# Kernel optimization log

Hardware: AMD Instinct MI355X
Metric: run time of the kernel (lower is better)

Reference implementation:

```python
import jax, jax.numpy as jnp
import numpy as np

NUM_HEADS = 8
EPS = 1e-9


def setup_inputs() -> dict:
    key = jax.random.key(0)
    ks = jax.random.split(key, 5)
    B, S, D = 2, 2048, 512
    x = jax.random.normal(ks[0], (B, S, D), dtype=jnp.float32)
    Wq = jax.random.normal(ks[1], (D, D), dtype=jnp.float32) * (1.0 / np.sqrt(D))
    Wk = jax.random.normal(ks[2], (D, D), dtype=jnp.float32) * (1.0 / np.sqrt(D))
    Wv = jax.random.normal(ks[3], (D, D), dtype=jnp.float32) * (1.0 / np.sqrt(D))
    Wo = jax.random.normal(ks[4], (D, D), dtype=jnp.float32) * (1.0 / np.sqrt(D))
    gamma = jnp.ones((D,), dtype=jnp.float32)
    beta = jnp.zeros((D,), dtype=jnp.float32)
    return {"x": x, "Wq": Wq, "Wk": Wk, "Wv": Wv, "Wo": Wo, "gamma": gamma, "beta": beta}


def _layernorm(x, gamma, beta):
    mean = jnp.mean(x, axis=-1, keepdims=True)
    var = jnp.mean(jnp.square(x - mean), axis=-1, keepdims=True)
    return gamma * ((x - mean) * jax.lax.rsqrt(var + EPS)) + beta


def reference(x, Wq, Wk, Wv, Wo, gamma, beta):
    B, S, D = x.shape
    H = NUM_HEADS
    dh = D // H
    # Note: in the original, K_V=(inputs, inputs) is captured BEFORE LayerNorm,
    # so only Q is layer-normalized; K and V use the raw inputs.
    q_in = _layernorm(x, gamma, beta)
    Q = jnp.einsum('bsd,de->bse', q_in, Wq).reshape(B, S, H, dh)
    K = jnp.einsum('bsd,de->bse', x, Wk).reshape(B, S, H, dh)
    V = jnp.einsum('bsd,de->bse', x, Wv).reshape(B, S, H, dh)
    # scaled dot-product attention (bias = 0, dropout disabled since dropout=1)
    scores = jnp.einsum('bqhd,bkhd->bhqk', Q, K) / jnp.sqrt(jnp.float32(dh))
    attn = jax.nn.softmax(scores, axis=-1)
    ctx = jnp.einsum('bhqk,bkhd->bqhd', attn, V).reshape(B, S, D)
    out = jnp.einsum('bsd,de->bse', ctx, Wo) + x  # output proj + residual
    return out
```

## Files before the change

### kernel.cpp

```cpp
#include <hip/hip_runtime.h>

typedef __bf16 bf16x8 __attribute__((ext_vector_type(8)));
typedef float f32x4 __attribute__((ext_vector_type(4)));

#define SCALE_LOG2E 0.18033688011112042f

__device__ __forceinline__ float bf2f(unsigned int u) { return __uint_as_float(u << 16); }
__device__ __forceinline__ unsigned short f2bfu(float f) {
    union { __bf16 h; unsigned short u; } v;
    v.h = (__bf16)f;
    return v.u;
}
__device__ __forceinline__ unsigned int pk2bf(float a, float b) {
    union { __bf16 h[2]; unsigned int u; } v;
    v.h[0] = (__bf16)a; v.h[1] = (__bf16)b;
    return v.u;
}

__device__ int probe_bf16(const void* xp) {
    const unsigned short* u = (const unsigned short*)xp;
    int cnt = 0;
    for (int i = 0; i < 128; i++) {
        unsigned e = (u[i] >> 7) & 0xFFu;
        cnt += (e == 0u || (e >= 0x6Cu && e <= 0x8Au)) ? 1 : 0;
    }
    return cnt >= 120;
}

__global__ __launch_bounds__(64)
void probe_k(const void* __restrict__ x, const void* __restrict__ Wq, int* __restrict__ flags) {
    if (threadIdx.x == 0) {
        flags[0] = probe_bf16(x);
        flags[1] = probe_bf16(Wq);
    }
}

__device__ __forceinline__ void load8f(const void* p, int isb, size_t idx, float* o) {
    if (isb) {
        uint4 v = *(const uint4*)((const unsigned short*)p + idx);
        o[0] = bf2f(v.x & 0xffffu); o[1] = bf2f(v.x >> 16);
        o[2] = bf2f(v.y & 0xffffu); o[3] = bf2f(v.y >> 16);
        o[4] = bf2f(v.z & 0xffffu); o[5] = bf2f(v.z >> 16);
        o[6] = bf2f(v.w & 0xffffu); o[7] = bf2f(v.w >> 16);
    } else {
        const float* f = (const float*)p + idx;
        float4 a = *(const float4*)f;
        float4 b = *(const float4*)(f + 4);
        o[0] = a.x; o[1] = a.y; o[2] = a.z; o[3] = a.w;
        o[4] = b.x; o[5] = b.y; o[6] = b.z; o[7] = b.w;
    }
}
__device__ __forceinline__ void load2f(const void* p, int isb, size_t idx, float& a, float& b) {
    if (isb) {
        unsigned int v = *(const unsigned int*)((const unsigned short*)p + idx);
        a = bf2f(v & 0xffffu); b = bf2f(v >> 16);
    } else {
        float2 f = *(const float2*)((const float*)p + idx);
        a = f.x; b = f.y;
    }
}
__device__ __forceinline__ float load1f(const void* p, int isb, size_t idx) {
    return isb ? bf2f((unsigned int)((const unsigned short*)p)[idx]) : ((const float*)p)[idx];
}

__global__ __launch_bounds__(256)
void setup_k(const void* __restrict__ x, const void* __restrict__ Wq, const void* __restrict__ Wk,
             const void* __restrict__ Wv, const void* __restrict__ Wo,
             const void* __restrict__ gamma, const void* __restrict__ beta,
             float* __restrict__ rowstats, float* __restrict__ gf, float* __restrict__ bfv,
             unsigned short* __restrict__ WT, const int* __restrict__ flags) {
    const int t = threadIdx.x;
    const int bid = blockIdx.x;
    if (bid < 1024) {
        const int isb = flags[1];
        __shared__ float tile[32][33];
        const int which = bid >> 8, tl = bid & 255;
        const int bx = (tl & 15) * 32, by = (tl >> 4) * 32;
        const void* W = (which == 0) ? Wq : (which == 1) ? Wk : (which == 2) ? Wv : Wo;
        unsigned short* dst = WT + (size_t)which * 512 * 512;
        const int xx = t & 31, y0 = t >> 5;
#pragma unroll
        for (int i = 0; i < 4; i++) {
            int y = y0 + i * 8;
            tile[y][xx] = load1f(W, isb, (size_t)(by + y) * 512 + bx + xx);
        }
        __syncthreads();
#pragma unroll
        for (int i = 0; i < 4; i++) {
            int y = y0 + i * 8;
            dst[(size_t)(bx + y) * 512 + by + xx] = f2bfu(tile[xx][y]);
        }
        return;
    }
    const int isb = flags[0];
    if (bid >= 5120) {
        const void* src = (bid == 5120) ? gamma : beta;
        float* dst = (bid == 5120) ? gf : bfv;
        float a, b;
        load2f(src, isb, (size_t)t * 2, a, b);
        dst[t * 2] = a; dst[t * 2 + 1] = b;
        return;
    }
    const int row = bid - 1024;
    float a, b;
    load2f(x, isb, (size_t)row * 512 + t * 2, a, b);
    float s = a + b, sq = a * a + b * b;
#pragma unroll
    for (int msk = 1; msk < 64; msk <<= 1) {
        s += __shfl_xor(s, msk);
        sq += __shfl_xor(sq, msk);
    }
    __shared__ float red[8];
    if ((t & 63) == 0) { red[t >> 6] = s; red[4 + (t >> 6)] = sq; }
    __syncthreads();
    if (t == 0) {
        float S = red[0] + red[1] + red[2] + red[3];
        float SQ = red[4] + red[5] + red[6] + red[7];
        float mean = S * (1.0f / 512.0f);
        float var = SQ * (1.0f / 512.0f) - mean * mean;
        rowstats[2 * row] = mean;
        rowstats[2 * row + 1] = rsqrtf(fmaxf(var, 0.0f) + 1e-9f);
    }
}

__global__ __launch_bounds__(256)
void proj_all_k(const void* __restrict__ x, const unsigned short* __restrict__ WT,
                const float* __restrict__ rowstats, const float* __restrict__ gf,
                const float* __restrict__ bfv, unsigned short* __restrict__ Qb,
                unsigned short* __restrict__ Kb, unsigned short* __restrict__ VtF,
                const int* __restrict__ flags) {
    __shared__ unsigned short As[128 * 40];
    __shared__ unsigned short Bs[128 * 40];
    __shared__ float Gs[512], Bts[512];
    const int t = threadIdx.x;
    const int isb = flags[0];
    const int w = t >> 6, lane = t & 63;
    const int quad = lane >> 4, ln = lane & 15;

    if (blockIdx.z == 0) {
        const int role = blockIdx.x & 1;
        const int n0 = (blockIdx.x >> 1) * 128;
        const int m0 = blockIdx.y * 128;
        const unsigned short* BT = WT + (size_t)role * 512 * 512;
        unsigned short* out = role ? Kb : Qb;
        const int wm = w & 1, wn = w >> 1;
        Gs[t] = gf[t]; Gs[t + 256] = gf[t + 256];
        Bts[t] = bfv[t]; Bts[t + 256] = bfv[t + 256];

        f32x4 acc[4][4];
        const f32x4 zero = {0.f, 0.f, 0.f, 0.f};
#pragma unroll
        for (int i = 0; i < 4; i++)
#pragma unroll
            for (int j = 0; j < 4; j++) acc[i][j] = zero;

        for (int kt = 0; kt < 512; kt += 32) {
            __syncthreads();
#pragma unroll
            for (int i = 0; i < 2; i++) {
                int o = t + i * 256;
                int r = o >> 2, c8 = o & 3;
                size_t gidx = (size_t)(m0 + r) * 512 + kt + c8 * 8;
                if (isb && role == 1) {
                    *(uint4*)(&As[r * 40 + c8 * 8]) = *(const uint4*)((const unsigned short*)x + gidx);
                } else {
                    float f[8];
                    load8f(x, isb, gidx, f);
                    if (role == 0) {
                        float mean = rowstats[2 * (m0 + r)];
                        float inv = rowstats[2 * (m0 + r) + 1];
#pragma unroll
                        for (int j = 0; j < 8; j++) {
                            int k = kt + c8 * 8 + j;
                            f[j] = (f[j] - mean) * inv * Gs[k] + Bts[k];
                        }
                    }
                    unsigned int pk[4];
#pragma unroll
                    for (int j = 0; j < 4; j++) pk[j] = pk2bf(f[2 * j], f[2 * j + 1]);
                    *(uint4*)(&As[r * 40 + c8 * 8]) = make_uint4(pk[0], pk[1], pk[2], pk[3]);
                }
                *(uint4*)(&Bs[r * 40 + c8 * 8]) = *(const uint4*)(BT + (size_t)(n0 + r) * 512 + kt + c8 * 8);
            }
            __syncthreads();
            bf16x8 af[4], bfr[4];
#pragma unroll
            for (int i = 0; i < 4; i++) {
                af[i] = *(const bf16x8*)(&As[(wm * 64 + i * 16 + ln) * 40 + quad * 8]);
                bfr[i] = *(const bf16x8*)(&Bs[(wn * 64 + i * 16 + ln) * 40 + quad * 8]);
            }
#pragma unroll
            for (int i = 0; i < 4; i++)
#pragma unroll
                for (int j = 0; j < 4; j++)
                    acc[i][j] = __builtin_amdgcn_mfma_f32_16x16x32_bf16(af[i], bfr[j], acc[i][j], 0, 0, 0);
        }
#pragma unroll
        for (int i = 0; i < 4; i++)
#pragma unroll
            for (int j = 0; j < 4; j++)
#pragma unroll
                for (int r = 0; r < 4; r++) {
                    int grow = m0 + wm * 64 + i * 16 + quad * 4 + r;
                    int gcol = n0 + wn * 64 + j * 16 + ln;
                    float v = acc[i][j][r];
                    if (role == 0) v *= SCALE_LOG2E;
                    out[(size_t)grow * 512 + gcol] = f2bfu(v);
                }
    } else {
        const int m0 = blockIdx.x * 64;
        const int n0 = blockIdx.y * 128;
        const unsigned short* AW = WT + (size_t)2 * 512 * 512;

        f32x4 acc[8];
        const f32x4 zero = {0.f, 0.f, 0.f, 0.f};
#pragma unroll
        for (int j = 0; j < 8; j++) acc[j] = zero;

        for (int kt = 0; kt < 512; kt += 32) {
            __syncthreads();
            {
                int r = t >> 2, c8 = t & 3;
                *(uint4*)(&As[r * 40 + c8 * 8]) = *(const uint4*)(AW + (size_t)(m0 + r) * 512 + kt + c8 * 8);
            }
#pragma unroll
            for (int i = 0; i < 2; i++) {
                int o = t + i * 256;
                int r = o >> 2, c8 = o & 3;
                size_t gidx = (size_t)(n0 + r) * 512 + kt + c8 * 8;
                if (isb) {
                    *(uint4*)(&Bs[r * 40 + c8 * 8]) = *(const uint4*)((const unsigned short*)x + gidx);
                } else {
                    float f[8];
                    load8f(x, isb, gidx, f);
                    unsigned int pk[4];
#pragma unroll
                    for (int j = 0; j < 4; j++) pk[j] = pk2bf(f[2 * j], f[2 * j + 1]);
                    *(uint4*)(&Bs[r * 40 + c8 * 8]) = make_uint4(pk[0], pk[1], pk[2], pk[3]);
                }
            }
            __syncthreads();
            bf16x8 af = *(const bf16x8*)(&As[(w * 16 + ln) * 40 + quad * 8]);
#pragma unroll
            for (int j = 0; j < 8; j++) {
                bf16x8 bfr = *(const bf16x8*)(&Bs[(j * 16 + ln) * 40 + quad * 8]);
                acc[j] = __builtin_amdgcn_mfma_f32_16x16x32_bf16(af, bfr, acc[j], 0, 0, 0);
            }
        }
#pragma unroll
        for (int j = 0; j < 8; j++)
#pragma unroll
            for (int r = 0; r < 4; r++) {
                int grow = m0 + w * 16 + quad * 4 + r;
                int gcol = n0 + j * 16 + ln;
                VtF[(size_t)grow * 4096 + gcol] = f2bfu(acc[j][r]);
            }
    }
}

__global__ __launch_bounds__(1024, 2)
void attn_m_k(const unsigned short* __restrict__ Qb, const unsigned short* __restrict__ Kb,
              const unsigned short* __restrict__ VtF, unsigned short* __restrict__ ctx) {
    const int S = 2048, PT = 72, NT = 32;
    const int t = threadIdx.x;
    const int qb = blockIdx.x, h = blockIdx.y, b = blockIdx.z;
    const int w = t >> 6, lane = t & 63;
    const int quad = lane >> 4, ln = lane & 15;
    const int qs = w & 3, kq = w >> 2;

    __shared__ unsigned short sh[32256];
    unsigned short* const Qs  = sh;
    unsigned short* const KsA = sh + 4608;
    unsigned short* const KsB = sh + 9216;
    unsigned short* const Vt0 = sh + 13824;
    unsigned short* const Vt1 = sh + 18432;
    unsigned short* const Vt2 = sh + 23040;
    unsigned short* const Vt3 = sh + 27648;

    const size_t baseQ  = (size_t)(b * S + qb * 64) * 512 + h * 64;
    const size_t baseK  = (size_t)(b * S) * 512 + h * 64;
    const size_t baseVt = (size_t)(h * 64) * 4096 + (size_t)b * S;

    const int r64 = (t & 511) >> 3, c8 = t & 7;

    const int stoff = r64 * PT + c8 * 8;
    const int kfo0  = (kq * 16 + ln) * PT + quad * 8;
    const int vto   = ln * PT + kq * 16 + quad * 4;

    const unsigned short* const gK = Kb + baseK + (size_t)r64 * 512 + c8 * 8;
    const unsigned short* const gV = VtF + baseVt + (size_t)r64 * 4096 + c8 * 8;

    uint4 sa, sb;
    if (t < 512) { sa = *(const uint4*)(gK); sb = *(const uint4*)(gK + 32768); }
    else         { sa = *(const uint4*)(gV); sb = *(const uint4*)(gV + 64); }

    if (t < 512)
        *(uint4*)(&Qs[stoff]) = *(const uint4*)(Qb + baseQ + (size_t)r64 * 512 + c8 * 8);
    __syncthreads();
    bf16x8 qf[2];
#pragma unroll
    for (int i = 0; i < 2; i++)
        qf[i] = *(const bf16x8*)(&Qs[(qs * 16 + ln) * PT + quad * 8 + 32 * i]);

    f32x4 acc[4];
    const f32x4 zero = {0.f, 0.f, 0.f, 0.f};
#pragma unroll
    for (int j = 0; j < 4; j++) acc[j] = zero;
    float lsum = 0.f;

#define STAGE(KS, VT, R)                                                    \
    {                                                                       \
        if (t < 512) *(uint4*)(&KS[stoff]) = R;                             \
        else         *(uint4*)(&VT[stoff]) = R;                             \
    }
#define PRELOAD(R, kt)                                                      \
    if ((kt) < NT) {                                                        \
        if (t < 512) R = *(const uint4*)(gK + (size_t)(kt) * 32768);        \
        else         R = *(const uint4*)(gV + (size_t)(kt) * 64);           \
    }
#define QK_EXP(KS, U0, U1)                                                  \
    {                                                                       \
        f32x4 sc = zero;                                                    \
        sc = __builtin_amdgcn_mfma_f32_16x16x32_bf16(                       \
            *(const bf16x8*)(&KS[kfo0]), qf[0], sc, 0, 0, 0);               \
        sc = __builtin_amdgcn_mfma_f32_16x16x32_bf16(                       \
            *(const bf16x8*)(&KS[kfo0 + 32]), qf[1], sc, 0, 0, 0);          \
        float e0 = __builtin_amdgcn_exp2f(fminf(sc[0], 30.f));              \
        float e1 = __builtin_amdgcn_exp2f(fminf(sc[1], 30.f));              \
        float e2 = __builtin_amdgcn_exp2f(fminf(sc[2], 30.f));              \
        float e3 = __builtin_amdgcn_exp2f(fminf(sc[3], 30.f));              \
        lsum += (e0 + e1) + (e2 + e3);                                      \
        U0 = pk2bf(e0, e1); U1 = pk2bf(e2, e3);                             \
    }
#define PV4(VTE, VTO)                                                       \
    {                                                                       \
        bf16x8 ap = __builtin_bit_cast(bf16x8, make_uint4(uA0, uA1, uB0, uB1)); \
        _Pragma("unroll")                                                   \
        for (int nt = 0; nt < 4; nt++) {                                    \
            uint2 ve = *(const uint2*)(&VTE[vto + nt * 16 * PT]);           \
            uint2 vo = *(const uint2*)(&VTO[vto + nt * 16 * PT]);           \
            bf16x8 vb = __builtin_bit_cast(bf16x8, make_uint4(ve.x, ve.y, vo.x, vo.y)); \
            acc[nt] = __builtin_amdgcn_mfma_f32_16x16x32_bf16(ap, vb, acc[nt], 0, 0, 0); \
        }                                                                   \
    }

    for (int m = 0; m < 8; m++) {
        const int T = m * 4;
        unsigned int uA0, uA1, uB0, uB1;
        STAGE(KsA, Vt0, sa);
        __syncthreads();
        PRELOAD(sa, T + 2);
        QK_EXP(KsA, uA0, uA1);
        STAGE(KsB, Vt1, sb);
        __syncthreads();
        PRELOAD(sb, T + 3);
        QK_EXP(KsB, uB0, uB1);
        PV4(Vt0, Vt1);
        __syncthreads();
        STAGE(KsA, Vt2, sa);
        __syncthreads();
        PRELOAD(sa, T + 4);
        QK_EXP(KsA, uA0, uA1);
        STAGE(KsB, Vt3, sb);
        __syncthreads();
        PRELOAD(sb, T + 5);
        QK_EXP(KsB, uB0, uB1);
        PV4(Vt2, Vt3);
        __syncthreads();
    }
#undef STAGE
#undef PRELOAD
#undef QK_EXP
#undef PV4

    lsum += __shfl_xor(lsum, 16);
    lsum += __shfl_xor(lsum, 32);

    float* scr  = (float*)sh;
    float* lred = scr + 13056;
    if (quad == 0) lred[kq * 64 + qs * 16 + ln] = lsum;
    if (kq != 0) {
        const int pb = (kq - 1) * 4352 + (qs * 16 + quad * 4) * 68 + ln;
#pragma unroll
        for (int nt = 0; nt < 4; nt++)
#pragma unroll
            for (int r = 0; r < 4; r++)
                scr[pb + r * 68 + nt * 16] = acc[nt][r];
    }
    __syncthreads();
    if (kq == 0) {
        const size_t baseO = (size_t)(b * S + qb * 64 + qs * 16 + quad * 4) * 512 + h * 64 + ln;
#pragma unroll
        for (int r = 0; r < 4; r++) {
            int qrow = qs * 16 + quad * 4 + r;
            float lt = lred[qrow] + lred[64 + qrow] + lred[128 + qrow] + lred[192 + qrow];
            float inv = 1.0f / lt;
            int rb = qrow * 68 + ln;
#pragma unroll
            for (int nt = 0; nt < 4; nt++) {
                float v = acc[nt][r] + scr[rb + nt * 16] + scr[4352 + rb + nt * 16] + scr[8704 + rb + nt * 16];
                ctx[baseO + (size_t)r * 512 + nt * 16] = f2bfu(v * inv);
            }
        }
    }
}

__global__ __launch_bounds__(256)
void outproj_k(const unsigned short* __restrict__ ctx, const unsigned short* __restrict__ BT,
               const void* __restrict__ x, void* __restrict__ outp, const int* __restrict__ flags) {
    __shared__ unsigned short As[128 * 40];
    __shared__ unsigned short Bs[64 * 40];
    const int t = threadIdx.x;
    const int isb = flags[0];
    const int m0 = blockIdx.y * 128, n0 = blockIdx.x * 64;
    const int w = t >> 6, lane = t & 63;
    const int wm = w & 1, wn = w >> 1;
    const int quad = lane >> 4, ln = lane & 15;

    f32x4 acc[4][2];
    const f32x4 zero = {0.f, 0.f, 0.f, 0.f};
#pragma unroll
    for (int i = 0; i < 4; i++)
#pragma unroll
        for (int j = 0; j < 2; j++) acc[i][j] = zero;

    for (int kt = 0; kt < 512; kt += 32) {
        __syncthreads();
#pragma unroll
        for (int i = 0; i < 2; i++) {
            int o = t + i * 256;
            int r = o >> 2, c8 = o & 3;
            *(uint4*)(&As[r * 40 + c8 * 8]) = *(const uint4*)(ctx + (size_t)(m0 + r) * 512 + kt + c8 * 8);
        }
        {
            int r = t >> 2, c8 = t & 3;
            *(uint4*)(&Bs[r * 40 + c8 * 8]) = *(const uint4*)(BT + (size_t)(n0 + r) * 512 + kt + c8 * 8);
        }
        __syncthreads();
        bf16x8 af[4], bfr[2];
#pragma unroll
        for (int i = 0; i < 4; i++)
            af[i] = *(const bf16x8*)(&As[(wm * 64 + i * 16 + ln) * 40 + quad * 8]);
#pragma unroll
        for (int j = 0; j < 2; j++)
            bfr[j] = *(const bf16x8*)(&Bs[(wn * 32 + j * 16 + ln) * 40 + quad * 8]);
#pragma unroll
        for (int i = 0; i < 4; i++)
#pragma unroll
            for (int j = 0; j < 2; j++)
                acc[i][j] = __builtin_amdgcn_mfma_f32_16x16x32_bf16(af[i], bfr[j], acc[i][j], 0, 0, 0);
    }
#pragma unroll
    for (int i = 0; i < 4; i++)
#pragma unroll
        for (int j = 0; j < 2; j++)
#pragma unroll
            for (int r = 0; r < 4; r++) {
                int grow = m0 + wm * 64 + i * 16 + quad * 4 + r;
                int gcol = n0 + wn * 32 + j * 16 + ln;
                size_t idx = (size_t)grow * 512 + gcol;
                float v = acc[i][j][r] + load1f(x, isb, idx);
                if (isb) ((unsigned short*)outp)[idx] = f2bfu(v);
                else     ((float*)outp)[idx] = v;
            }
}

__global__ __launch_bounds__(256)
void fill_k(unsigned short* out, int n) {
    int i = blockIdx.x * 256 + threadIdx.x;
    if (i < n) out[i] = 0x4442;
}

extern "C" void kernel_launch(void* const* d_in, const int* in_sizes, int n_in,
                              void* d_out, int out_size, void* d_ws, size_t ws_size,
                              hipStream_t stream) {
    const void* x     = d_in[0];
    const void* Wq    = d_in[1];
    const void* Wk    = d_in[2];
    const void* Wv    = d_in[3];
    const void* Wo    = d_in[4];
    const void* gamma = d_in[5];
    const void* beta  = d_in[6];

    const size_t NW = 512 * 512;
    const size_t NX = 4096 * 512;
    char* w = (char*)d_ws;

    const size_t FULL_STATS_OFF = 2097152 + 3 * NX * 2;
    const size_t NEED_FULL = FULL_STATS_OFF + 32768 + 4096 + 16;

    if (ws_size < NEED_FULL) {
        fill_k<<<(out_size + 255) / 256, 256, 0, stream>>>((unsigned short*)d_out, out_size);
        return;
    }

    unsigned short* WT  = (unsigned short*)w;
    unsigned short* Qb  = (unsigned short*)(w + 2097152);
    unsigned short* Kb  = Qb + NX;
    unsigned short* VtF = Kb + NX;
    unsigned short* ctx = Qb;
    float* rowstats = (float*)(w + FULL_STATS_OFF);
    float* gf = rowstats + 8192;
    float* bfv = gf + 512;
    int* flags = (int*)(bfv + 512);

    probe_k<<<1, 64, 0, stream>>>(x, Wq, flags);
    setup_k<<<5122, 256, 0, stream>>>(x, Wq, Wk, Wv, Wo, gamma, beta, rowstats, gf, bfv, WT, flags);
    proj_all_k<<<dim3(8, 32, 2), 256, 0, stream>>>(x, WT, rowstats, gf, bfv, Qb, Kb, VtF, flags);
    attn_m_k<<<dim3(32, 8, 2), 1024, 0, stream>>>(Qb, Kb, VtF, ctx);
    outproj_k<<<dim3(8, 32), 256, 0, stream>>>(ctx, WT + 3 * NW, x, d_out, flags);
}
```

Baseline: 165.4 us.

## Halve attention block to 512 threads with two query subtiles per wave

```diff
diff --git a/kernel.cpp b/kernel.cpp
--- a/kernel.cpp
+++ b/kernel.cpp
@@ -258,7 +258,7 @@
     }
 }
 
-__global__ __launch_bounds__(1024, 2)
+__global__ __launch_bounds__(512, 4)
 void attn_m_k(const unsigned short* __restrict__ Qb, const unsigned short* __restrict__ Kb,
               const unsigned short* __restrict__ VtF, unsigned short* __restrict__ ctx) {
     const int S = 2048, PT = 72, NT = 32;
@@ -266,7 +266,7 @@
     const int qb = blockIdx.x, h = blockIdx.y, b = blockIdx.z;
     const int w = t >> 6, lane = t & 63;
     const int quad = lane >> 4, ln = lane & 15;
-    const int qs = w & 3, kq = w >> 2;
+    const int kq = w & 3, qh = w >> 2;
 
     __shared__ unsigned short sh[32256];
     unsigned short* const Qs  = sh;
@@ -281,90 +281,119 @@
     const size_t baseK  = (size_t)(b * S) * 512 + h * 64;
     const size_t baseVt = (size_t)(h * 64) * 4096 + (size_t)b * S;
 
-    const int r64 = (t & 511) >> 3, c8 = t & 7;
-
-    const int stoff = r64 * PT + c8 * 8;
-    const int kfo0  = (kq * 16 + ln) * PT + quad * 8;
-    const int vto   = ln * PT + kq * 16 + quad * 4;
-
-    const unsigned short* const gK = Kb + baseK + (size_t)r64 * 512 + c8 * 8;
-    const unsigned short* const gV = VtF + baseVt + (size_t)r64 * 4096 + c8 * 8;
-
-    uint4 sa, sb;
-    if (t < 512) { sa = *(const uint4*)(gK); sb = *(const uint4*)(gK + 32768); }
-    else         { sa = *(const uint4*)(gV); sb = *(const uint4*)(gV + 64); }
-
-    if (t < 512)
-        *(uint4*)(&Qs[stoff]) = *(const uint4*)(Qb + baseQ + (size_t)r64 * 512 + c8 * 8);
+    const int c8 = t & 7;
+    const int isK = t < 256;
+    const int rS = (t & 255) >> 3;
+    const int stoff0 = rS * PT + c8 * 8;
+    const int stoff1 = (rS + 32) * PT + c8 * 8;
+
+    const int kfo0 = (kq * 16 + ln) * PT + quad * 8;
+    const int vto  = ln * PT + kq * 16 + quad * 4;
+
+    const unsigned short* const gK = Kb + baseK + (size_t)rS * 512 + c8 * 8;
+    const unsigned short* const gV = VtF + baseVt + (size_t)rS * 4096 + c8 * 8;
+
+    uint4 sa0, sa1, sb0, sb1;
+    if (isK) {
+        sa0 = *(const uint4*)(gK);          sa1 = *(const uint4*)(gK + 16384);
+        sb0 = *(const uint4*)(gK + 32768);  sb1 = *(const uint4*)(gK + 49152);
+    } else {
+        sa0 = *(const uint4*)(gV);          sa1 = *(const uint4*)(gV + 131072);
+        sb0 = *(const uint4*)(gV + 64);     sb1 = *(const uint4*)(gV + 64 + 131072);
+    }
+
+    {
+        const int rQ = t >> 3;
+        *(uint4*)(&Qs[rQ * PT + c8 * 8]) = *(const uint4*)(Qb + baseQ + (size_t)rQ * 512 + c8 * 8);
+    }
     __syncthreads();
-    bf16x8 qf[2];
-#pragma unroll
-    for (int i = 0; i < 2; i++)
-        qf[i] = *(const bf16x8*)(&Qs[(qs * 16 + ln) * PT + quad * 8 + 32 * i]);
-
-    f32x4 acc[4];
+    bf16x8 qf[2][2];
+#pragma unroll
+    for (int s2 = 0; s2 < 2; s2++)
+#pragma unroll
+        for (int i = 0; i < 2; i++)
+            qf[s2][i] = *(const bf16x8*)(&Qs[(qh * 32 + s2 * 16 + ln) * PT + quad * 8 + 32 * i]);
+
+    f32x4 acc[2][4];
     const f32x4 zero = {0.f, 0.f, 0.f, 0.f};
 #pragma unroll
-    for (int j = 0; j < 4; j++) acc[j] = zero;
-    float lsum = 0.f;
-
-#define STAGE(KS, VT, R)                                                    \
+    for (int s2 = 0; s2 < 2; s2++)
+#pragma unroll
+        for (int j = 0; j < 4; j++) acc[s2][j] = zero;
+    float lsum0 = 0.f, lsum1 = 0.f;
+
+#define STAGE(KS, VT, R0, R1)                                               \
     {                                                                       \
-        if (t < 512) *(uint4*)(&KS[stoff]) = R;                             \
-        else         *(uint4*)(&VT[stoff]) = R;                             \
-    }
-#define PRELOAD(R, kt)                                                      \
+        if (isK) { *(uint4*)(&KS[stoff0]) = R0; *(uint4*)(&KS[stoff1]) = R1; } \
+        else     { *(uint4*)(&VT[stoff0]) = R0; *(uint4*)(&VT[stoff1]) = R1; } \
+    }
+#define PRELOAD(R0, R1, kt)                                                 \
     if ((kt) < NT) {                                                        \
-        if (t < 512) R = *(const uint4*)(gK + (size_t)(kt) * 32768);        \
-        else         R = *(const uint4*)(gV + (size_t)(kt) * 64);           \
-    }
-#define QK_EXP(KS, U0, U1)                                                  \
+        if (isK) {                                                          \
+            R0 = *(const uint4*)(gK + (size_t)(kt) * 32768);                \
+            R1 = *(const uint4*)(gK + (size_t)(kt) * 32768 + 16384);        \
+        } else {                                                            \
+            R0 = *(const uint4*)(gV + (size_t)(kt) * 64);                   \
+            R1 = *(const uint4*)(gV + (size_t)(kt) * 64 + 131072);          \
+        }                                                                   \
+    }
+#define QK_EXP(KS, U00, U01, U10, U11)                                      \
     {                                                                       \
-        f32x4 sc = zero;                                                    \
-        sc = __builtin_amdgcn_mfma_f32_16x16x32_bf16(                       \
-            *(const bf16x8*)(&KS[kfo0]), qf[0], sc, 0, 0, 0);               \
-        sc = __builtin_amdgcn_mfma_f32_16x16x32_bf16(                       \
-            *(const bf16x8*)(&KS[kfo0 + 32]), qf[1], sc, 0, 0, 0);          \
-        float e0 = __builtin_amdgcn_exp2f(fminf(sc[0], 30.f));              \
-        float e1 = __builtin_amdgcn_exp2f(fminf(sc[1], 30.f));              \
-        float e2 = __builtin_amdgcn_exp2f(fminf(sc[2], 30.f));              \
-        float e3 = __builtin_amdgcn_exp2f(fminf(sc[3], 30.f));              \
-        lsum += (e0 + e1) + (e2 + e3);                                      \
-        U0 = pk2bf(e0, e1); U1 = pk2bf(e2, e3);                             \
+        bf16x8 kf0 = *(const bf16x8*)(&KS[kfo0]);                           \
+        bf16x8 kf1 = *(const bf16x8*)(&KS[kfo0 + 32]);                      \
+        f32x4 sc0 = zero, sc1 = zero;                                       \
+        sc0 = __builtin_amdgcn_mfma_f32_16x16x32_bf16(kf0, qf[0][0], sc0, 0, 0, 0); \
+        sc0 = __builtin_amdgcn_mfma_f32_16x16x32_bf16(kf1, qf[0][1], sc0, 0, 0, 0); \
+        sc1 = __builtin_amdgcn_mfma_f32_16x16x32_bf16(kf0, qf[1][0], sc1, 0, 0, 0); \
+        sc1 = __builtin_amdgcn_mfma_f32_16x16x32_bf16(kf1, qf[1][1], sc1, 0, 0, 0); \
+        float a0 = __builtin_amdgcn_exp2f(fminf(sc0[0], 30.f));             \
+        float a1 = __builtin_amdgcn_exp2f(fminf(sc0[1], 30.f));             \
+        float a2 = __builtin_amdgcn_exp2f(fminf(sc0[2], 30.f));             \
+        float a3 = __builtin_amdgcn_exp2f(fminf(sc0[3], 30.f));             \
+        lsum0 += (a0 + a1) + (a2 + a3);                                     \
+        U00 = pk2bf(a0, a1); U01 = pk2bf(a2, a3);                           \
+        float b0 = __builtin_amdgcn_exp2f(fminf(sc1[0], 30.f));             \
+        float b1 = __builtin_amdgcn_exp2f(fminf(sc1[1], 30.f));             \
+        float b2 = __builtin_amdgcn_exp2f(fminf(sc1[2], 30.f));             \
+        float b3 = __builtin_amdgcn_exp2f(fminf(sc1[3], 30.f));             \
+        lsum1 += (b0 + b1) + (b2 + b3);                                     \
+        U10 = pk2bf(b0, b1); U11 = pk2bf(b2, b3);                           \
     }
 #define PV4(VTE, VTO)                                                       \
     {                                                                       \
-        bf16x8 ap = __builtin_bit_cast(bf16x8, make_uint4(uA0, uA1, uB0, uB1)); \
+        bf16x8 ap0 = __builtin_bit_cast(bf16x8, make_uint4(uA00, uA01, uB00, uB01)); \
+        bf16x8 ap1 = __builtin_bit_cast(bf16x8, make_uint4(uA10, uA11, uB10, uB11)); \
         _Pragma("unroll")                                                   \
         for (int nt = 0; nt < 4; nt++) {                                    \
             uint2 ve = *(const uint2*)(&VTE[vto + nt * 16 * PT]);           \
             uint2 vo = *(const uint2*)(&VTO[vto + nt * 16 * PT]);           \
             bf16x8 vb = __builtin_bit_cast(bf16x8, make_uint4(ve.x, ve.y, vo.x, vo.y)); \
-            acc[nt] = __builtin_amdgcn_mfma_f32_16x16x32_bf16(ap, vb, acc[nt], 0, 0, 0); \
+            acc[0][nt] = __builtin_amdgcn_mfma_f32_16x16x32_bf16(ap0, vb, acc[0][nt], 0, 0, 0); \
+            acc[1][nt] = __builtin_amdgcn_mfma_f32_16x16x32_bf16(ap1, vb, acc[1][nt], 0, 0, 0); \
         }                                                                   \
     }
 
     for (int m = 0; m < 8; m++) {
         const int T = m * 4;
-        unsigned int uA0, uA1, uB0, uB1;
-        STAGE(KsA, Vt0, sa);
-        __syncthreads();
-        PRELOAD(sa, T + 2);
-        QK_EXP(KsA, uA0, uA1);
-        STAGE(KsB, Vt1, sb);
-        __syncthreads();
-        PRELOAD(sb, T + 3);
-        QK_EXP(KsB, uB0, uB1);
+        unsigned int uA00, uA01, uA10, uA11, uB00, uB01, uB10, uB11;
+        STAGE(KsA, Vt0, sa0, sa1);
+        __syncthreads();
+        PRELOAD(sa0, sa1, T + 2);
+        QK_EXP(KsA, uA00, uA01, uA10, uA11);
+        STAGE(KsB, Vt1, sb0, sb1);
+        __syncthreads();
+        PRELOAD(sb0, sb1, T + 3);
+        QK_EXP(KsB, uB00, uB01, uB10, uB11);
         PV4(Vt0, Vt1);
         __syncthreads();
-        STAGE(KsA, Vt2, sa);
-        __syncthreads();
-        PRELOAD(sa, T + 4);
-        QK_EXP(KsA, uA0, uA1);
-        STAGE(KsB, Vt3, sb);
-        __syncthreads();
-        PRELOAD(sb, T + 5);
-        QK_EXP(KsB, uB0, uB1);
+        STAGE(KsA, Vt2, sa0, sa1);
+        __syncthreads();
+        PRELOAD(sa0, sa1, T + 4);
+        QK_EXP(KsA, uA00, uA01, uA10, uA11);
+        STAGE(KsB, Vt3, sb0, sb1);
+        __syncthreads();
+        PRELOAD(sb0, sb1, T + 5);
+        QK_EXP(KsB, uB00, uB01, uB10, uB11);
         PV4(Vt2, Vt3);
         __syncthreads();
     }
@@ -373,33 +402,44 @@
 #undef QK_EXP
 #undef PV4
 
-    lsum += __shfl_xor(lsum, 16);
-    lsum += __shfl_xor(lsum, 32);
-
+    lsum0 += __shfl_xor(lsum0, 16);
+    lsum0 += __shfl_xor(lsum0, 32);
+    lsum1 += __shfl_xor(lsum1, 16);
+    lsum1 += __shfl_xor(lsum1, 32);
+
+    __syncthreads();
     float* scr  = (float*)sh;
     float* lred = scr + 13056;
-    if (quad == 0) lred[kq * 64 + qs * 16 + ln] = lsum;
+    if (quad == 0) {
+        lred[kq * 64 + qh * 32 + ln] = lsum0;
+        lred[kq * 64 + qh * 32 + 16 + ln] = lsum1;
+    }
     if (kq != 0) {
-        const int pb = (kq - 1) * 4352 + (qs * 16 + quad * 4) * 68 + ln;
-#pragma unroll
-        for (int nt = 0; nt < 4; nt++)
-#pragma unroll
-            for (int r = 0; r < 4; r++)
-                scr[pb + r * 68 + nt * 16] = acc[nt][r];
+        const int pb = (kq - 1) * 4352 + (qh * 32 + quad * 4) * 68 + ln;
+#pragma unroll
+        for (int s2 = 0; s2 < 2; s2++)
+#pragma unroll
+            for (int nt = 0; nt < 4; nt++)
+#pragma unroll
+                for (int r = 0; r < 4; r++)
+                    scr[pb + (s2 * 16 + r) * 68 + nt * 16] = acc[s2][nt][r];
     }
     __syncthreads();
     if (kq == 0) {
-        const size_t baseO = (size_t)(b * S + qb * 64 + qs * 16 + quad * 4) * 512 + h * 64 + ln;
-#pragma unroll
-        for (int r = 0; r < 4; r++) {
-            int qrow = qs * 16 + quad * 4 + r;
-            float lt = lred[qrow] + lred[64 + qrow] + lred[128 + qrow] + lred[192 + qrow];
-            float inv = 1.0f / lt;
-            int rb = qrow * 68 + ln;
-#pragma unroll
-            for (int nt = 0; nt < 4; nt++) {
-                float v = acc[nt][r] + scr[rb + nt * 16] + scr[4352 + rb + nt * 16] + scr[8704 + rb + nt * 16];
-                ctx[baseO + (size_t)r * 512 + nt * 16] = f2bfu(v * inv);
+#pragma unroll
+        for (int s2 = 0; s2 < 2; s2++) {
+            const size_t baseO = (size_t)(b * S + qb * 64 + qh * 32 + s2 * 16 + quad * 4) * 512 + h * 64 + ln;
+#pragma unroll
+            for (int r = 0; r < 4; r++) {
+                int qrow = qh * 32 + s2 * 16 + quad * 4 + r;
+                float lt = lred[qrow] + lred[64 + qrow] + lred[128 + qrow] + lred[192 + qrow];
+                float inv = 1.0f / lt;
+                int rb = qrow * 68 + ln;
+#pragma unroll
+                for (int nt = 0; nt < 4; nt++) {
+                    float v = acc[s2][nt][r] + scr[rb + nt * 16] + scr[4352 + rb + nt * 16] + scr[8704 + rb + nt * 16];
+                    ctx[baseO + (size_t)r * 512 + nt * 16] = f2bfu(v * inv);
+                }
             }
         }
     }
@@ -507,6 +547,6 @@
     probe_k<<<1, 64, 0, stream>>>(x, Wq, flags);
     setup_k<<<5122, 256, 0, stream>>>(x, Wq, Wk, Wv, Wo, gamma, beta, rowstats, gf, bfv, WT, flags);
     proj_all_k<<<dim3(8, 32, 2), 256, 0, stream>>>(x, WT, rowstats, gf, bfv, Qb, Kb, VtF, flags);
-    attn_m_k<<<dim3(32, 8, 2), 1024, 0, stream>>>(Qb, Kb, VtF, ctx);
+    attn_m_k<<<dim3(32, 8, 2), 512, 0, stream>>>(Qb, Kb, VtF, ctx);
     outproj_k<<<dim3(8, 32), 256, 0, stream>>>(ctx, WT + 3 * NW, x, d_out, flags);
 }
```

Result: no change. 162.8 us (-1.6%).
